# Performance work log

Measured on AMD Instinct MI355X. Metric: run time of the kernel, lower is better.

Reference implementation:

```python
import jax, jax.numpy as jnp
import numpy as np

B, D = 32768, 512
ANCHOR_CLASS = 0  # module starts with self.a = 0; labels guarantee >1 sample of class 0


def setup_inputs() -> dict:
    key = jax.random.key(0)
    k0, k1, k2, k3, k4 = jax.random.split(key, 5)
    return {
        "label": jax.random.randint(k0, (B,), 0, 7, dtype=jnp.int64),
        "p_t": jax.random.normal(k1, (B, D), dtype=jnp.float32),
        "p_a": jax.random.normal(k2, (B, D), dtype=jnp.float32),
        "s_t": jax.random.normal(k3, (B, D), dtype=jnp.float32),
        "s_a": jax.random.normal(k4, (B, D), dtype=jnp.float32),
    }


def _modality_loss(X, anchor_idx, pos_mask, neg_mask):
    # cosine similarity of every row vs. the anchor row, fully vectorized
    anchor = X[anchor_idx]                                 # [D]
    dots = X @ anchor                                      # [B]
    cos = dots / (jnp.linalg.norm(X, axis=1) * jnp.linalg.norm(anchor))
    pos_cnt = jnp.sum(pos_mask)
    neg_cnt = jnp.sum(neg_mask)
    pos_score = jnp.where(pos_cnt > 0,
                          jnp.sum(jnp.where(pos_mask, cos, 0.0)) / jnp.maximum(pos_cnt, 1),
                          0.0)
    neg_score = jnp.where(neg_cnt > 0,
                          jnp.sum(jnp.where(neg_mask, cos, 0.0)) / jnp.maximum(neg_cnt, 1),
                          0.0)
    return 2.0 - pos_score + neg_score


def reference(label, p_t, p_a, s_t, s_a):
    a = ANCHOR_CLASS
    is_class = (label == a)
    # deterministic anchor: first sample of the anchor class (original draws one
    # uniformly; any member gives the same math structure)
    anchor_idx = jnp.argmax(is_class)
    not_anchor = jnp.arange(label.shape[0]) != anchor_idx
    pos_mask = is_class & not_anchor
    neg_mask = (~is_class) & not_anchor

    losses = jnp.stack([
        _modality_loss(p_t, anchor_idx, pos_mask, neg_mask),
        _modality_loss(p_a, anchor_idx, pos_mask, neg_mask),
        _modality_loss(s_t, anchor_idx, pos_mask, neg_mask),
        _modality_loss(s_a, anchor_idx, pos_mask, neg_mask),
    ])
    return jnp.mean(losses)
```

## Files before the change

kernel.cpp:

```cpp
#include <hip/hip_runtime.h>

#define B_ROWS   32768
#define D_DIM    512
#define NBLOCKS  2048
#define TPB      256
#define NWAVES   (NBLOCKS * (TPB / 64))
#define RPW      (B_ROWS / NWAVES)

struct Ws {
    unsigned anchor_idx;
    int      cnt0;
};

__device__ __forceinline__ float dot4(float4 a, float4 b) {
    return a.x * b.x + a.y * b.y + a.z * b.z + a.w * b.w;
}

__device__ __forceinline__ float fold_reduce8(const float v[8], int lane) {
    float w[4];
    #pragma unroll
    for (int i = 0; i < 4; ++i) {
        float send = (lane & 32) ? v[i] : v[i + 4];
        float rcv  = __shfl_xor(send, 32);
        w[i] = ((lane & 32) ? v[i + 4] : v[i]) + rcv;
    }
    float u[2];
    #pragma unroll
    for (int i = 0; i < 2; ++i) {
        float send = (lane & 16) ? w[i] : w[i + 2];
        float rcv  = __shfl_xor(send, 16);
        u[i] = ((lane & 16) ? w[i + 2] : w[i]) + rcv;
    }
    float t;
    {
        float send = (lane & 8) ? u[0] : u[1];
        float rcv  = __shfl_xor(send, 8);
        t = ((lane & 8) ? u[1] : u[0]) + rcv;
    }
    t += __shfl_xor(t, 4);
    t += __shfl_xor(t, 2);
    t += __shfl_xor(t, 1);
    return t;
}

__global__ void scan_labels_kernel(const int* __restrict__ label, Ws* ws) {
    int tid = blockIdx.x * blockDim.x + threadIdx.x;
    const int4* L4 = (const int4*)label;
    int4 v = L4[tid];
    int cnt = (v.x == 0) + (v.y == 0) + (v.z == 0) + (v.w == 0);
    unsigned base = (unsigned)tid * 4;
    unsigned mymin = 0xFFFFFFFFu;
    if (v.w == 0) mymin = base + 3;
    if (v.z == 0) mymin = base + 2;
    if (v.y == 0) mymin = base + 1;
    if (v.x == 0) mymin = base;
    for (int off = 32; off; off >>= 1) {
        cnt += __shfl_xor(cnt, off);
        unsigned o = (unsigned)__shfl_xor((int)mymin, off);
        mymin = mymin < o ? mymin : o;
    }
    if ((threadIdx.x & 63) == 0) {
        if (cnt) atomicAdd(&ws->cnt0, cnt);
        if (mymin != 0xFFFFFFFFu) atomicMin(&ws->anchor_idx, mymin);
    }
}

__launch_bounds__(TPB, 6)
__global__ void cos_accum_kernel(const int* __restrict__ label,
                                 const float* __restrict__ p_t,
                                 const float* __restrict__ p_a,
                                 const float* __restrict__ s_t,
                                 const float* __restrict__ s_a,
                                 const Ws* __restrict__ ws,
                                 float* __restrict__ partials) {
    const float* X[4] = {p_t, p_a, s_t, s_a};
    __shared__ float4 anc4[4 * 128];
    __shared__ float  red[TPB / 64][8];

    const unsigned aidx = ws->anchor_idx;
    const int lane = threadIdx.x & 63;
    const int wid  = threadIdx.x >> 6;
    const int gwave = blockIdx.x * (TPB / 64) + wid;

    for (int idx = threadIdx.x; idx < 4 * 128; idx += TPB) {
        anc4[idx] = ((const float4*)(X[idx >> 7] + (size_t)aidx * D_DIM))[idx & 127];
    }
    __syncthreads();

    float inv_mine;
    {
        float va[8];
        #pragma unroll
        for (int m = 0; m < 4; ++m) {
            float4 a0 = anc4[(m << 7) + lane];
            float4 a1 = anc4[(m << 7) + 64 + lane];
            va[m]     = dot4(a0, a0) + dot4(a1, a1);
            va[m + 4] = 0.f;
        }
        inv_mine = rsqrtf(fold_reduce8(va, lane));
    }

    float posAcc = 0.f, negAcc = 0.f;

    #pragma unroll
    for (int k = 0; k < RPW; ++k) {
        unsigned r = (unsigned)gwave + (unsigned)k * NWAVES;
        int lab = label[__builtin_amdgcn_readfirstlane((int)r)];

        float4 x[8];
        #pragma unroll
        for (int m = 0; m < 4; ++m) {
            const float4* Xr = (const float4*)(X[m]) + (size_t)r * (D_DIM / 4);
            x[2 * m]     = Xr[lane];
            x[2 * m + 1] = Xr[64 + lane];
        }

        float v[8];
        #pragma unroll
        for (int m = 0; m < 4; ++m) {
            float4 b0 = anc4[(m << 7) + lane];
            float4 b1 = anc4[(m << 7) + 64 + lane];
            v[m]     = dot4(x[2 * m], b0)       + dot4(x[2 * m + 1], b1);
            v[m + 4] = dot4(x[2 * m], x[2 * m]) + dot4(x[2 * m + 1], x[2 * m + 1]);
        }
        float t     = fold_reduce8(v, lane);
        float other = __shfl_xor(t, 32);
        if (((lane & 39) == 0) && (r != aidx)) {
            float c = t * rsqrtf(other) * inv_mine;
            if (lab == 0) posAcc += c; else negAcc += c;
        }
    }

    if ((lane & 39) == 0) {
        int m = lane >> 3;
        red[wid][m]     = posAcc;
        red[wid][4 + m] = negAcc;
    }
    __syncthreads();
    if (threadIdx.x < 8) {
        int j = threadIdx.x;
        partials[blockIdx.x * 8 + j] = red[0][j] + red[1][j] + red[2][j] + red[3][j];
    }
}

__global__ void finalize_kernel(const Ws* __restrict__ ws,
                                const float* __restrict__ partials,
                                float* __restrict__ out) {
    __shared__ float red[256];
    int t = threadIdx.x;
    int j = t & 7;
    float s = 0.f;
    for (int r = t >> 3; r < NBLOCKS; r += 32)
        s += partials[r * 8 + j];
    red[t] = s;
    __syncthreads();
    if (t < 8) {
        float tot = 0.f;
        #pragma unroll
        for (int k = 0; k < 32; ++k) tot += red[k * 8 + t];
        red[t] = tot;
    }
    __syncthreads();
    if (t == 0) {
        float pos_cnt = (float)ws->cnt0;
        float neg_cnt = (float)(B_ROWS - (ws->cnt0 + 1));
        float total = 0.f;
        #pragma unroll
        for (int m = 0; m < 4; ++m) {
            float ps = (pos_cnt > 0.f) ? red[m]     / fmaxf(pos_cnt, 1.f) : 0.f;
            float ns = (neg_cnt > 0.f) ? red[4 + m] / fmaxf(neg_cnt, 1.f) : 0.f;
            total += 2.0f - ps + ns;
        }
        out[0] = total * 0.25f;
    }
}

extern "C" void kernel_launch(void* const* d_in, const int* in_sizes, int n_in,
                              void* d_out, int out_size, void* d_ws, size_t ws_size,
                              hipStream_t stream) {
    const int*   label = (const int*)  d_in[0];
    const float* p_t   = (const float*)d_in[1];
    const float* p_a   = (const float*)d_in[2];
    const float* s_t   = (const float*)d_in[3];
    const float* s_a   = (const float*)d_in[4];
    Ws* ws = (Ws*)d_ws;
    float* partials = (float*)d_ws + 64;

    hipMemsetAsync(d_ws, 0xFF, 8, stream);

    scan_labels_kernel <<<32,      TPB, 0, stream>>>(label, ws);
    cos_accum_kernel   <<<NBLOCKS, TPB, 0, stream>>>(label, p_t, p_a, s_t, s_a, ws, partials);
    finalize_kernel    <<<1,       TPB, 0, stream>>>(ws, partials, (float*)d_out);
}
```

Before: 71.34 us.

## Double-buffer row loads via global_load_lds DMA with fewer persistent blocks

Cuts the grid to 512 blocks with 16 rows per wave and streams each row into a per-wave double-buffered LDS area using direct global-to-LDS loads. Explicit vmcnt waits overlap the next row's fetch with the current row's dot products. The anchor row moves into registers and the labels are prefetched. It trades occupancy (launch bounds 2) and relies on hand-counted vmcnt waits being correct, for fewer blocks and deeper explicit prefetch on this memory-bound kernel.

```diff
diff --git a/kernel.cpp b/kernel.cpp
--- a/kernel.cpp
+++ b/kernel.cpp
@@ -1,16 +1,40 @@
 #include <hip/hip_runtime.h>
+#include <cstdint>
 
 #define B_ROWS   32768
 #define D_DIM    512
-#define NBLOCKS  2048
+#define NBLOCKS  512
 #define TPB      256
-#define NWAVES   (NBLOCKS * (TPB / 64))
+#define WPB      (TPB / 64)
+#define NWAVES   (NBLOCKS * WPB)
 #define RPW      (B_ROWS / NWAVES)
 
 struct Ws {
     unsigned anchor_idx;
     int      cnt0;
 };
+
+#define WAITVM(N) do { asm volatile("s_waitcnt vmcnt(" #N ")" ::: "memory"); \
+                       __builtin_amdgcn_sched_barrier(0); } while (0)
+
+typedef __attribute__((address_space(3))) unsigned int lds_u32;
+typedef const __attribute__((address_space(1))) unsigned int glb_u32;
+
+__device__ __forceinline__ void dma1k(const float* src, const float4* dst) {
+    __builtin_amdgcn_global_load_lds((glb_u32*)(uintptr_t)src,
+                                     (lds_u32*)(unsigned int)(uintptr_t)dst,
+                                     16, 0, 0);
+}
+
+__device__ __forceinline__ void dma_row(const float* const X[4], unsigned r,
+                                        const float4* dstbase, int lane) {
+    #pragma unroll
+    for (int m = 0; m < 4; ++m) {
+        const float* src = X[m] + (size_t)r * D_DIM + lane * 4;
+        dma1k(src,       dstbase + m * 128);
+        dma1k(src + 256, dstbase + m * 128 + 64);
+    }
+}
 
 __device__ __forceinline__ float dot4(float4 a, float4 b) {
     return a.x * b.x + a.y * b.y + a.z * b.z + a.w * b.w;
@@ -65,7 +89,7 @@
     }
 }
 
-__launch_bounds__(TPB, 6)
+__launch_bounds__(TPB, 2)
 __global__ void cos_accum_kernel(const int* __restrict__ label,
                                  const float* __restrict__ p_t,
                                  const float* __restrict__ p_a,
@@ -74,27 +98,34 @@
                                  const Ws* __restrict__ ws,
                                  float* __restrict__ partials) {
     const float* X[4] = {p_t, p_a, s_t, s_a};
-    __shared__ float4 anc4[4 * 128];
-    __shared__ float  red[TPB / 64][8];
+    __shared__ float4 buf[WPB][2][512];
+    __shared__ float  red[WPB][8];
 
     const unsigned aidx = ws->anchor_idx;
     const int lane = threadIdx.x & 63;
-    const int wid  = threadIdx.x >> 6;
-    const int gwave = blockIdx.x * (TPB / 64) + wid;
-
-    for (int idx = threadIdx.x; idx < 4 * 128; idx += TPB) {
-        anc4[idx] = ((const float4*)(X[idx >> 7] + (size_t)aidx * D_DIM))[idx & 127];
-    }
-    __syncthreads();
+    const int wid  = __builtin_amdgcn_readfirstlane((int)(threadIdx.x >> 6));
+    const unsigned gwave = (unsigned)blockIdx.x * WPB + (unsigned)wid;
+
+    float4 an[8];
+    #pragma unroll
+    for (int m = 0; m < 4; ++m) {
+        const float4* A = (const float4*)(X[m] + (size_t)aidx * D_DIM);
+        an[2 * m]     = A[lane];
+        an[2 * m + 1] = A[64 + lane];
+    }
+    dma_row(X, gwave,          &buf[wid][0][0], lane);
+    dma_row(X, gwave + NWAVES, &buf[wid][1][0], lane);
+
+    int lab[RPW];
+    #pragma unroll
+    for (int k = 0; k < RPW; ++k) lab[k] = label[gwave + (unsigned)k * NWAVES];
 
     float inv_mine;
     {
         float va[8];
         #pragma unroll
         for (int m = 0; m < 4; ++m) {
-            float4 a0 = anc4[(m << 7) + lane];
-            float4 a1 = anc4[(m << 7) + 64 + lane];
-            va[m]     = dot4(a0, a0) + dot4(a1, a1);
+            va[m]     = dot4(an[2 * m], an[2 * m]) + dot4(an[2 * m + 1], an[2 * m + 1]);
             va[m + 4] = 0.f;
         }
         inv_mine = rsqrtf(fold_reduce8(va, lane));
@@ -104,30 +135,33 @@
 
     #pragma unroll
     for (int k = 0; k < RPW; ++k) {
-        unsigned r = (unsigned)gwave + (unsigned)k * NWAVES;
-        int lab = label[__builtin_amdgcn_readfirstlane((int)r)];
+        if (k < RPW - 1) { WAITVM(8); }
+        else            { WAITVM(0); }
+
+        const unsigned r = gwave + (unsigned)k * NWAVES;
+        const float4* bp = &buf[wid][k & 1][0];
 
         float4 x[8];
         #pragma unroll
         for (int m = 0; m < 4; ++m) {
-            const float4* Xr = (const float4*)(X[m]) + (size_t)r * (D_DIM / 4);
-            x[2 * m]     = Xr[lane];
-            x[2 * m + 1] = Xr[64 + lane];
-        }
-
+            x[2 * m]     = bp[m * 128 + lane];
+            x[2 * m + 1] = bp[m * 128 + 64 + lane];
+        }
         float v[8];
         #pragma unroll
         for (int m = 0; m < 4; ++m) {
-            float4 b0 = anc4[(m << 7) + lane];
-            float4 b1 = anc4[(m << 7) + 64 + lane];
-            v[m]     = dot4(x[2 * m], b0)       + dot4(x[2 * m + 1], b1);
-            v[m + 4] = dot4(x[2 * m], x[2 * m]) + dot4(x[2 * m + 1], x[2 * m + 1]);
-        }
+            v[m]     = dot4(x[2 * m], an[2 * m]) + dot4(x[2 * m + 1], an[2 * m + 1]);
+            v[m + 4] = dot4(x[2 * m], x[2 * m])  + dot4(x[2 * m + 1], x[2 * m + 1]);
+        }
+
+        if (k + 2 < RPW)
+            dma_row(X, gwave + (unsigned)(k + 2) * NWAVES, &buf[wid][k & 1][0], lane);
+
         float t     = fold_reduce8(v, lane);
         float other = __shfl_xor(t, 32);
         if (((lane & 39) == 0) && (r != aidx)) {
             float c = t * rsqrtf(other) * inv_mine;
-            if (lab == 0) posAcc += c; else negAcc += c;
+            if (lab[k] == 0) posAcc += c; else negAcc += c;
         }
     }
 
```

Result: faster. 61.26 us (-14.1%).
